# Optimization experiments

Hardware: AMD Instinct MI355X
Metric: run time of the kernel (lower is better)

The kernel has to match this reference:

```python
import jax, jax.numpy as jnp
import numpy as np

H = 16       # num_attention_heads
HKV = 4      # num_key_value_heads
HD = 128     # head_dim
G = H // HKV # num_key_value_groups


def setup_inputs() -> dict:
    key = jax.random.key(0)
    ks = jax.random.split(key, 7)
    s = 0.02
    B, S, D = 2, 2048, 2048
    return {
        "hidden_states": jax.random.normal(ks[0], (B, S, D), jnp.float32),
        "Wq": jax.random.normal(ks[1], (D, H * HD), jnp.float32) * s,
        "Wk": jax.random.normal(ks[2], (D, HKV * HD), jnp.float32) * s,
        "Wv": jax.random.normal(ks[3], (D, HKV * HD), jnp.float32) * s,
        "Wg": jax.random.normal(ks[4], (H * HD, HKV), jnp.float32) * s,
        "Wd": jax.random.normal(ks[5], (HKV * HD, HKV), jnp.float32) * s,
        "Wo": jax.random.normal(ks[6], (H * HD, D), jnp.float32) * s,
    }


def reference(hidden_states, Wq, Wk, Wv, Wg, Wd, Wo):
    b, s, _ = hidden_states.shape
    scale = HD ** -0.5

    q_flat = hidden_states @ Wq                    # [b,s,H*HD]
    k_flat = hidden_states @ Wk                    # [b,s,HKV*HD]
    v_flat = hidden_states @ Wv                    # [b,s,HKV*HD]

    gate = q_flat @ Wg                             # [b,s,HKV] (per query pos)
    delta = v_flat @ Wd                            # [b,s,HKV] (per key pos)
    # attn_bias: [b,HKV,key_len] after transpose; broadcast over query dim
    bias = (jax.nn.sigmoid(gate) * delta).transpose(0, 2, 1)  # [b,HKV,s]

    # [b,HKV,G,s,HD] query grouped by kv-head; [b,HKV,s,HD] key/value
    q = q_flat.reshape(b, s, HKV, G, HD).transpose(0, 2, 3, 1, 4)
    k = k_flat.reshape(b, s, HKV, HD).transpose(0, 2, 1, 3)
    v = v_flat.reshape(b, s, HKV, HD).transpose(0, 2, 1, 3)

    scores = jnp.einsum('bngqd,bnkd->bngqk', q, k) * scale  # [b,HKV,G,s,s]
    logits = scores + bias[:, :, None, None, :]

    causal = jnp.tril(jnp.ones((s, s), dtype=bool))
    # 'relu' mask: key positions allowed only where relu(bias) > 0
    allowed = causal[None, None, None] & (bias > 0)[:, :, None, None, :]
    neg = jnp.finfo(logits.dtype).min
    logits = jnp.where(allowed, logits, neg)

    p = jax.nn.softmax(logits, axis=-1)
    o = jnp.einsum('bngqk,bnkd->bngqd', p, v)               # [b,HKV,G,s,HD]
    o = o.transpose(0, 3, 1, 2, 4).reshape(b, s, H * HD)
    return o @ Wo
```

## Files before the change

kernel.cpp:

```cpp
#include <hip/hip_runtime.h>
#include <hip/hip_bf16.h>
#include <cmath>
#include <cstdint>

typedef __attribute__((ext_vector_type(8))) short short8;
typedef __attribute__((ext_vector_type(4))) float floatx4;
typedef __attribute__((ext_vector_type(4))) unsigned int uintx4;

typedef const __attribute__((address_space(1))) unsigned int* gas_p;
typedef __attribute__((address_space(3))) unsigned int* las_p;

#define LOG2E 1.4426950408889634f

__device__ inline unsigned short f2bf(float f) {
  unsigned int u = __builtin_bit_cast(unsigned int, f);
  unsigned int r = (u + 0x7FFFu + ((u >> 16) & 1u)) >> 16;
  return (unsigned short)r;
}
__device__ inline float bf2f(unsigned short h) {
  unsigned int u = ((unsigned int)h) << 16;
  return __builtin_bit_cast(float, u);
}

__global__ void k_f32_to_bf16(const float* __restrict__ in, unsigned short* __restrict__ out, int n4) {
  int i = blockIdx.x * 256 + threadIdx.x;
  if (i >= n4) return;
  float4 v = reinterpret_cast<const float4*>(in)[i];
  uint2 o;
  o.x = (unsigned)f2bf(v.x) | ((unsigned)f2bf(v.y) << 16);
  o.y = (unsigned)f2bf(v.z) | ((unsigned)f2bf(v.w) << 16);
  reinterpret_cast<uint2*>(out)[i] = o;
}

__global__ void k_transpose_w(const float* __restrict__ in, unsigned short* __restrict__ out,
                              int K, int N, float scl) {
  __shared__ float t[32][33];
  int n0 = blockIdx.x * 32, k0 = blockIdx.y * 32;
  int tx = threadIdx.x & 31, ty = threadIdx.x >> 5;
  #pragma unroll
  for (int r = ty; r < 32; r += 8)
    t[r][tx] = in[(long)(k0 + r) * N + n0 + tx];
  __syncthreads();
  #pragma unroll
  for (int r = ty; r < 32; r += 8)
    out[(long)(n0 + r) * K + k0 + tx] = f2bf(t[tx][r] * scl);
}

__global__ void k_wproj(const float* __restrict__ W, const float* __restrict__ Ws,
                        float* __restrict__ out, int Kw) {
  int d = blockIdx.x;
  float a0 = 0, a1 = 0, a2 = 0, a3 = 0;
  for (int j = threadIdx.x; j < Kw; j += 256) {
    float w = W[(long)d * Kw + j];
    float4 g = reinterpret_cast<const float4*>(Ws)[j];
    a0 += w * g.x; a1 += w * g.y; a2 += w * g.z; a3 += w * g.w;
  }
  #pragma unroll
  for (int off = 1; off < 64; off <<= 1) {
    a0 += __shfl_xor(a0, off, 64); a1 += __shfl_xor(a1, off, 64);
    a2 += __shfl_xor(a2, off, 64); a3 += __shfl_xor(a3, off, 64);
  }
  __shared__ float red[4][4];
  if ((threadIdx.x & 63) == 0) {
    int wv = threadIdx.x >> 6;
    red[wv][0] = a0; red[wv][1] = a1; red[wv][2] = a2; red[wv][3] = a3;
  }
  __syncthreads();
  if (threadIdx.x < 4) {
    int nn = threadIdx.x;
    out[d * 4 + nn] = red[0][nn] + red[1][nn] + red[2][nn] + red[3][nn];
  }
}

__global__ void k_bias(const float* __restrict__ hs, const float* __restrict__ Wqg,
                       const float* __restrict__ Wvd, float* __restrict__ bias) {
  int row = blockIdx.x;
  int b = row >> 11, s = row & 2047;
  float g0 = 0, g1 = 0, g2 = 0, g3 = 0, d0 = 0, d1 = 0, d2 = 0, d3 = 0;
  const float* h = hs + (long)row * 2048;
  for (int j = threadIdx.x; j < 2048; j += 256) {
    float x = h[j];
    float4 a = reinterpret_cast<const float4*>(Wqg)[j];
    float4 c = reinterpret_cast<const float4*>(Wvd)[j];
    g0 += x * a.x; g1 += x * a.y; g2 += x * a.z; g3 += x * a.w;
    d0 += x * c.x; d1 += x * c.y; d2 += x * c.z; d3 += x * c.w;
  }
  #pragma unroll
  for (int off = 1; off < 64; off <<= 1) {
    g0 += __shfl_xor(g0, off, 64); g1 += __shfl_xor(g1, off, 64);
    g2 += __shfl_xor(g2, off, 64); g3 += __shfl_xor(g3, off, 64);
    d0 += __shfl_xor(d0, off, 64); d1 += __shfl_xor(d1, off, 64);
    d2 += __shfl_xor(d2, off, 64); d3 += __shfl_xor(d3, off, 64);
  }
  __shared__ float red[4][8];
  if ((threadIdx.x & 63) == 0) {
    int wv = threadIdx.x >> 6;
    red[wv][0] = g0; red[wv][1] = g1; red[wv][2] = g2; red[wv][3] = g3;
    red[wv][4] = d0; red[wv][5] = d1; red[wv][6] = d2; red[wv][7] = d3;
  }
  __syncthreads();
  if (threadIdx.x < 4) {
    int nn = threadIdx.x;
    float gg = red[0][nn] + red[1][nn] + red[2][nn] + red[3][nn];
    float dd = red[0][4 + nn] + red[1][4 + nn] + red[2][4 + nn] + red[3][4 + nn];
    float sig = 1.0f / (1.0f + __expf(-gg));
    float v = sig * dd;
    bias[(b * 4 + nn) * 2048 + s] = (v > 0.0f) ? v * LOG2E : -INFINITY;
  }
}

template <int WRITE_BF16>
__global__ __launch_bounds__(256, 2) void k_gemm_bt(
    const unsigned short* __restrict__ A, const unsigned short* __restrict__ Bt,
    void* __restrict__ Cout, int M, int N, int K) {
  __shared__ __align__(16) unsigned short As[128 * 32];
  __shared__ __align__(16) unsigned short Bs[128 * 32];
  const int tid = threadIdx.x;
  const int lane = tid & 63, wave = tid >> 6;
  const int quad = lane >> 4, l16 = lane & 15;
  const long bm = (long)blockIdx.y * 128, bn = (long)blockIdx.x * 128;
  const int wm = (wave >> 1) * 64, wn = (wave & 1) * 64;

  const floatx4 fz = {0.f, 0.f, 0.f, 0.f};
  floatx4 acc[4][4];
  #pragma unroll
  for (int i = 0; i < 4; i++)
    #pragma unroll
    for (int j = 0; j < 4; j++) acc[i][j] = fz;

  const int r0 = tid >> 2, c0 = (tid & 3) * 8;
  const unsigned short* Ag = A + (bm + r0) * K + c0;
  const unsigned short* Bg = Bt + (bn + r0) * K + c0;
  unsigned short* AsW0 = As + (wave * 16) * 32;
  unsigned short* AsW1 = As + (wave * 16 + 64) * 32;
  unsigned short* BsW0 = Bs + (wave * 16) * 32;
  unsigned short* BsW1 = Bs + (wave * 16 + 64) * 32;

  for (int kt = 0; kt < K; kt += 32) {
    __syncthreads();
    __builtin_amdgcn_global_load_lds((gas_p)(const void*)(Ag + kt),
                                     (las_p)(void*)AsW0, 16, 0, 0);
    __builtin_amdgcn_global_load_lds((gas_p)(const void*)(Ag + (long)64 * K + kt),
                                     (las_p)(void*)AsW1, 16, 0, 0);
    __builtin_amdgcn_global_load_lds((gas_p)(const void*)(Bg + kt),
                                     (las_p)(void*)BsW0, 16, 0, 0);
    __builtin_amdgcn_global_load_lds((gas_p)(const void*)(Bg + (long)64 * K + kt),
                                     (las_p)(void*)BsW1, 16, 0, 0);
    __syncthreads();
    short8 af[4], bf[4];
    #pragma unroll
    for (int i = 0; i < 4; i++)
      af[i] = *reinterpret_cast<const short8*>(&As[(wm + i * 16 + l16) * 32 + quad * 8]);
    #pragma unroll
    for (int j = 0; j < 4; j++)
      bf[j] = *reinterpret_cast<const short8*>(&Bs[(wn + j * 16 + l16) * 32 + quad * 8]);
    #pragma unroll
    for (int i = 0; i < 4; i++)
      #pragma unroll
      for (int j = 0; j < 4; j++)
        acc[i][j] = __builtin_amdgcn_mfma_f32_16x16x32_bf16(af[i], bf[j], acc[i][j], 0, 0, 0);
  }
  #pragma unroll
  for (int i = 0; i < 4; i++)
    #pragma unroll
    for (int j = 0; j < 4; j++)
      #pragma unroll
      for (int r = 0; r < 4; r++) {
        const long row = bm + wm + i * 16 + quad * 4 + r;
        const long col = bn + wn + j * 16 + l16;
        const float v = acc[i][j][r];
        if (WRITE_BF16)
          ((unsigned short*)Cout)[row * N + col] = f2bf(v);
        else
          ((float*)Cout)[row * N + col] = v;
      }
}

__global__ void k_transpose_v(const unsigned short* __restrict__ qkv, unsigned short* __restrict__ vt) {
  __shared__ unsigned short t[32][33];
  int c0 = blockIdx.x * 32, s0 = blockIdx.y * 32, b = blockIdx.z;
  int tx = threadIdx.x & 31, ty = threadIdx.x >> 5;
  #pragma unroll
  for (int r = ty; r < 32; r += 8)
    t[r][tx] = qkv[((long)(b * 2048 + s0 + r)) * 3072 + 2560 + c0 + tx];
  __syncthreads();
  #pragma unroll
  for (int r = ty; r < 32; r += 8)
    vt[((long)(b * 512 + c0 + r)) * 2048 + s0 + tx] = t[tx][r];
}

__global__ void k_vmean2(const unsigned short* __restrict__ vT, float* __restrict__ vmean) {
  const int row = blockIdx.x;
  const int tid = threadIdx.x, lane = tid & 63, wave = tid >> 6;
  uintx4 v = reinterpret_cast<const uintx4*>(vT + (long)row * 2048)[tid];
  float s = 0.f;
  #pragma unroll
  for (int i = 0; i < 4; i++) {
    unsigned u = v[i];
    s += bf2f((unsigned short)(u & 0xffff)) + bf2f((unsigned short)(u >> 16));
  }
  #pragma unroll
  for (int off = 1; off < 64; off <<= 1) s += __shfl_xor(s, off, 64);
  __shared__ float red[4];
  if (lane == 0) red[wave] = s;
  __syncthreads();
  if (tid == 0) vmean[row] = (red[0] + red[1] + red[2] + red[3]) * (1.0f / 2048.0f);
}

__global__ __launch_bounds__(256, 3) void k_attn(
    const unsigned short* __restrict__ qkv,
    const float* __restrict__ biasb,
    const unsigned short* __restrict__ vT,
    const float* __restrict__ vmean,
    unsigned short* __restrict__ o)
{
  int idx = blockIdx.x;
  const int g = idx & 3;
  const int n = (idx >> 2) & 3;
  const int b = (idx >> 4) & 1;
  const int qt = 31 - (idx >> 5);
  const int tid = threadIdx.x, lane = tid & 63, wave = tid >> 6;
  const int quad = lane >> 4, l16 = lane & 15;
  const int q0 = qt * 64 + wave * 16;

  __shared__ __align__(16) unsigned short Ks[64 * 144];
  __shared__ __align__(16) unsigned short Vs[128 * 72];
  __shared__ __align__(16) unsigned short Ps[4 * 16 * 72];
  unsigned short* Psw = Ps + wave * 1152;

  short8 qf[4];
  {
    const unsigned short* qp = qkv + (long)(b * 2048) * 3072 + (n * 4 + g) * 128;
    #pragma unroll
    for (int ks = 0; ks < 4; ks++)
      qf[ks] = *reinterpret_cast<const short8*>(
          qp + (long)(q0 + l16) * 3072 + ks * 32 + quad * 8);
  }

  const floatx4 fz = {0.f, 0.f, 0.f, 0.f};
  floatx4 oacc[8];
  #pragma unroll
  for (int j = 0; j < 8; j++) oacc[j] = fz;
  float mrow = -INFINITY, lrow = 0.0f;

  const float* biasrow = biasb + (b * 4 + n) * 2048;
  const unsigned short* kbase = qkv + (long)(b * 2048) * 3072 + 2048 + n * 128;
  const unsigned short* vbase = vT + (long)(b * 512 + n * 128) * 2048;
  const int kk_ = tid >> 4, hdo_ = (tid & 15) * 8;
  const int hd_ = tid >> 3, ko_ = (tid & 7) * 8;

  uintx4 kreg[4], vreg[4];
  float4 breg[4];
  {
    const unsigned short* kp = kbase;
    const unsigned short* vp = vbase;
    #pragma unroll
    for (int it = 0; it < 4; it++)
      kreg[it] = *reinterpret_cast<const uintx4*>(kp + (long)(kk_ + it * 16) * 3072 + hdo_);
    #pragma unroll
    for (int it = 0; it < 4; it++)
      vreg[it] = *reinterpret_cast<const uintx4*>(vp + (long)(hd_ + it * 32) * 2048 + ko_);
    #pragma unroll
    for (int kt = 0; kt < 4; kt++)
      breg[kt] = *reinterpret_cast<const float4*>(biasrow + kt * 16 + quad * 4);
  }

  const int kend = qt * 64 + 64;
  for (int k0 = 0; k0 < kend; k0 += 64) {
    __syncthreads();
    #pragma unroll
    for (int it = 0; it < 4; it++)
      *reinterpret_cast<uintx4*>(&Ks[(kk_ + it * 16) * 144 + hdo_]) = kreg[it];
    #pragma unroll
    for (int it = 0; it < 4; it++)
      *reinterpret_cast<uintx4*>(&Vs[(hd_ + it * 32) * 72 + ko_]) = vreg[it];
    float4 bcur[4];
    #pragma unroll
    for (int kt = 0; kt < 4; kt++) bcur[kt] = breg[kt];

    if (k0 + 64 < kend) {
      const unsigned short* kp = kbase + (long)(k0 + 64) * 3072;
      const unsigned short* vp = vbase + (k0 + 64);
      #pragma unroll
      for (int it = 0; it < 4; it++)
        kreg[it] = *reinterpret_cast<const uintx4*>(kp + (long)(kk_ + it * 16) * 3072 + hdo_);
      #pragma unroll
      for (int it = 0; it < 4; it++)
        vreg[it] = *reinterpret_cast<const uintx4*>(vp + (long)(hd_ + it * 32) * 2048 + ko_);
      #pragma unroll
      for (int kt = 0; kt < 4; kt++)
        breg[kt] = *reinterpret_cast<const float4*>(biasrow + (k0 + 64) + kt * 16 + quad * 4);
    }
    __syncthreads();

    const bool active = (k0 <= q0 + 15);
    if (active) {
      floatx4 sacc[4];
      #pragma unroll
      for (int kt = 0; kt < 4; kt++)
        sacc[kt] = (floatx4){bcur[kt].x, bcur[kt].y, bcur[kt].z, bcur[kt].w};
      #pragma unroll
      for (int ks = 0; ks < 4; ks++) {
        short8 kf[4];
        #pragma unroll
        for (int kt = 0; kt < 4; kt++)
          kf[kt] = *reinterpret_cast<const short8*>(&Ks[(kt * 16 + l16) * 144 + ks * 32 + quad * 8]);
        #pragma unroll
        for (int kt = 0; kt < 4; kt++)
          sacc[kt] = __builtin_amdgcn_mfma_f32_16x16x32_bf16(kf[kt], qf[ks], sacc[kt], 0, 0, 0);
      }

      const bool full = (k0 + 63 <= q0);
      if (!full) {
        const int diff = (q0 + l16) - (k0 + quad * 4);
        #pragma unroll
        for (int kt = 0; kt < 4; kt++)
          #pragma unroll
          for (int r = 0; r < 4; r++)
            if (kt * 16 + r > diff) sacc[kt][r] = -INFINITY;
      }
      float mx = -INFINITY;
      #pragma unroll
      for (int kt = 0; kt < 4; kt++)
        #pragma unroll
        for (int r = 0; r < 4; r++) mx = fmaxf(mx, sacc[kt][r]);
      mx = fmaxf(mx, __shfl_xor(mx, 16, 64));
      mx = fmaxf(mx, __shfl_xor(mx, 32, 64));
      const float mn = fmaxf(mrow, mx);
      const float mnc = fmaxf(mn, -1e38f);
      const float alpha = __builtin_amdgcn_exp2f(mrow - mnc);
      float rs = 0.0f;
      unsigned pk[4][2];
      #pragma unroll
      for (int kt = 0; kt < 4; kt++) {
        #pragma unroll
        for (int r = 0; r < 4; r++) {
          float p = __builtin_amdgcn_exp2f(sacc[kt][r] - mnc);
          sacc[kt][r] = p;
          rs += p;
        }
        #pragma unroll
        for (int r2 = 0; r2 < 2; r2++)
          pk[kt][r2] = (unsigned)f2bf(sacc[kt][2 * r2]) | ((unsigned)f2bf(sacc[kt][2 * r2 + 1]) << 16);
      }
      rs += __shfl_xor(rs, 16, 64);
      rs += __shfl_xor(rs, 32, 64);
      mrow = mn;
      lrow = lrow * alpha + rs;

      float al[4];
      #pragma unroll
      for (int r = 0; r < 4; r++) al[r] = __shfl(alpha, quad * 4 + r, 64);
      #pragma unroll
      for (int j = 0; j < 8; j++)
        #pragma unroll
        for (int r = 0; r < 4; r++) oacc[j][r] *= al[r];

      unsigned* Pd = reinterpret_cast<unsigned*>(Psw);
      #pragma unroll
      for (int kt = 0; kt < 4; kt++)
        #pragma unroll
        for (int r2 = 0; r2 < 2; r2++)
          Pd[l16 * 36 + kt * 8 + quad * 2 + r2] = pk[kt][r2];

      #pragma unroll
      for (int ks2 = 0; ks2 < 2; ks2++) {
        short8 pf = *reinterpret_cast<const short8*>(&Psw[l16 * 72 + ks2 * 32 + quad * 8]);
        #pragma unroll
        for (int j = 0; j < 8; j++) {
          short8 vf = *reinterpret_cast<const short8*>(&Vs[(j * 16 + l16) * 72 + ks2 * 32 + quad * 8]);
          oacc[j] = __builtin_amdgcn_mfma_f32_16x16x32_bf16(pf, vf, oacc[j], 0, 0, 0);
        }
      }
    }
  }

  const long obase = (long)(b * 2048) * 2048 + (n * 4 + g) * 128;
  #pragma unroll
  for (int r = 0; r < 4; r++) {
    const int qrow = q0 + quad * 4 + r;
    const float l = __shfl(lrow, quad * 4 + r, 64);
    const float inv = (l > 0.0f) ? 1.0f / l : 0.0f;
    #pragma unroll
    for (int j = 0; j < 8; j++) {
      const int hd = j * 16 + l16;
      float v = oacc[j][r] * inv;
      if (l <= 0.0f) v = vmean[(b * 4 + n) * 128 + hd];
      o[obase + (long)qrow * 2048 + hd] = f2bf(v);
    }
  }
}

extern "C" void kernel_launch(void* const* d_in, const int* in_sizes, int n_in,
                              void* d_out, int out_size, void* d_ws, size_t ws_size,
                              hipStream_t stream) {
  const float* hs = (const float*)d_in[0];
  const float* Wq = (const float*)d_in[1];
  const float* Wk = (const float*)d_in[2];
  const float* Wv = (const float*)d_in[3];
  const float* Wg = (const float*)d_in[4];
  const float* Wd = (const float*)d_in[5];
  const float* Wo = (const float*)d_in[6];
  float* out = (float*)d_out;

  char* ws = (char*)d_ws;
  unsigned short* hsb   = (unsigned short*)(ws);
  unsigned short* Wcomb = (unsigned short*)(ws + 16777216);
  unsigned short* Wot   = (unsigned short*)(ws + 29360128);
  float*  Wqg   = (float*)(ws + 37748736);
  float*  Wvd   = (float*)(ws + 37781504);
  float*  biasb = (float*)(ws + 37814272);
  unsigned short* qkv = (unsigned short*)(ws + 37879808);
  unsigned short* vT  = (unsigned short*)(ws + 63045632);
  float*  vmean = (float*)(ws + 67239936);
  unsigned short* ob  = (unsigned short*)(ws + 67244032);

  const float QSCALE = 0.08838834764831845f * LOG2E;

  k_f32_to_bf16<<<2097152 / 256, 256, 0, stream>>>(hs, hsb, 2097152);

  {
    dim3 g1(2048 / 32, 2048 / 32);
    dim3 g2(512 / 32, 2048 / 32);
    k_transpose_w<<<g1, 256, 0, stream>>>(Wq, Wcomb, 2048, 2048, QSCALE);
    k_transpose_w<<<g2, 256, 0, stream>>>(Wk, Wcomb + (long)2048 * 2048, 2048, 512, 1.0f);
    k_transpose_w<<<g2, 256, 0, stream>>>(Wv, Wcomb + (long)2560 * 2048, 2048, 512, 1.0f);
    k_transpose_w<<<g1, 256, 0, stream>>>(Wo, Wot, 2048, 2048, 1.0f);
  }

  k_wproj<<<2048, 256, 0, stream>>>(Wq, Wg, Wqg, 2048);
  k_wproj<<<2048, 256, 0, stream>>>(Wv, Wd, Wvd, 512);

  k_bias<<<4096, 256, 0, stream>>>(hs, Wqg, Wvd, biasb);

  {
    dim3 gq(3072 / 128, 4096 / 128);
    k_gemm_bt<1><<<gq, 256, 0, stream>>>(hsb, Wcomb, qkv, 4096, 3072, 2048);
  }

  {
    dim3 gv(16, 64, 2);
    k_transpose_v<<<gv, 256, 0, stream>>>(qkv, vT);
  }

  k_vmean2<<<1024, 256, 0, stream>>>(vT, vmean);

  k_attn<<<1024, 256, 0, stream>>>(qkv, biasb, vT, vmean, ob);

  {
    dim3 go(2048 / 128, 4096 / 128);
    k_gemm_bt<0><<<go, 256, 0, stream>>>(ob, Wot, out, 4096, 2048, 2048);
  }
}
```

Measured before the change: 344.4 us.

## Merge prep kernels and enlarge attention blocks to 128 query rows

Folds the four weight-transpose launches into one kernel and the two weight-projection launches into another. It also fuses the fp32-to-bf16 conversion of hidden states into the bias kernel so hidden states are read once. The attention kernel now uses 512-thread blocks of 8 waves covering 128 query rows, sharing each K/V tile load across twice as many waves and changing the K shared-memory padding. The risk is more idle waves per block on causal diagonal tiles, and register pressure under the new launch bounds.

```diff
diff --git a/kernel.cpp b/kernel.cpp
--- a/kernel.cpp
+++ b/kernel.cpp
@@ -22,33 +22,37 @@
   return __builtin_bit_cast(float, u);
 }
 
-__global__ void k_f32_to_bf16(const float* __restrict__ in, unsigned short* __restrict__ out, int n4) {
-  int i = blockIdx.x * 256 + threadIdx.x;
-  if (i >= n4) return;
-  float4 v = reinterpret_cast<const float4*>(in)[i];
-  uint2 o;
-  o.x = (unsigned)f2bf(v.x) | ((unsigned)f2bf(v.y) << 16);
-  o.y = (unsigned)f2bf(v.z) | ((unsigned)f2bf(v.w) << 16);
-  reinterpret_cast<uint2*>(out)[i] = o;
-}
-
-__global__ void k_transpose_w(const float* __restrict__ in, unsigned short* __restrict__ out,
-                              int K, int N, float scl) {
+__global__ void k_transpose_all(const float* __restrict__ Wq, const float* __restrict__ Wk,
+                                const float* __restrict__ Wv, const float* __restrict__ Wo,
+                                unsigned short* __restrict__ Wcomb, unsigned short* __restrict__ Wot,
+                                float qscale) {
   __shared__ float t[32][33];
-  int n0 = blockIdx.x * 32, k0 = blockIdx.y * 32;
-  int tx = threadIdx.x & 31, ty = threadIdx.x >> 5;
+  int id = blockIdx.x;
+  const float* src; unsigned short* dst; int N; float scl = 1.0f;
+  if (id < 4096)        { src = Wq; dst = Wcomb;                     N = 2048; scl = qscale; }
+  else if (id < 5120)   { src = Wk; dst = Wcomb + (long)2048 * 2048; N = 512;  id -= 4096; }
+  else if (id < 6144)   { src = Wv; dst = Wcomb + (long)2560 * 2048; N = 512;  id -= 5120; }
+  else                  { src = Wo; dst = Wot;                       N = 2048; id -= 6144; }
+  const int tilesX = N >> 5;
+  const int n0 = (id % tilesX) * 32, k0 = (id / tilesX) * 32;
+  const int tx = threadIdx.x & 31, ty = threadIdx.x >> 5;
   #pragma unroll
   for (int r = ty; r < 32; r += 8)
-    t[r][tx] = in[(long)(k0 + r) * N + n0 + tx];
+    t[r][tx] = src[(long)(k0 + r) * N + n0 + tx];
   __syncthreads();
   #pragma unroll
   for (int r = ty; r < 32; r += 8)
-    out[(long)(n0 + r) * K + k0 + tx] = f2bf(t[tx][r] * scl);
-}
-
-__global__ void k_wproj(const float* __restrict__ W, const float* __restrict__ Ws,
-                        float* __restrict__ out, int Kw) {
-  int d = blockIdx.x;
+    dst[(long)(n0 + r) * 2048 + k0 + tx] = f2bf(t[tx][r] * scl);
+}
+
+__global__ void k_wproj2(const float* __restrict__ Wq, const float* __restrict__ Wg,
+                         const float* __restrict__ Wv, const float* __restrict__ Wd,
+                         float* __restrict__ Wqg, float* __restrict__ Wvd) {
+  const int which = blockIdx.x >> 11, d = blockIdx.x & 2047;
+  const float* W  = which ? Wv : Wq;
+  const float* Ws = which ? Wd : Wg;
+  float* out      = which ? Wvd : Wqg;
+  const int Kw    = which ? 512 : 2048;
   float a0 = 0, a1 = 0, a2 = 0, a3 = 0;
   for (int j = threadIdx.x; j < Kw; j += 256) {
     float w = W[(long)d * Kw + j];
@@ -72,14 +76,27 @@
   }
 }
 
-__global__ void k_bias(const float* __restrict__ hs, const float* __restrict__ Wqg,
-                       const float* __restrict__ Wvd, float* __restrict__ bias) {
-  int row = blockIdx.x;
-  int b = row >> 11, s = row & 2047;
+__global__ void k_biascvt(const float* __restrict__ hs, const float* __restrict__ Wqg,
+                          const float* __restrict__ Wvd, unsigned short* __restrict__ hsb,
+                          float* __restrict__ bias) {
+  const int row = blockIdx.x;
+  const int b = row >> 11, s = row & 2047;
+  const int tid = threadIdx.x;
+  const float* h = hs + (long)row * 2048;
+  float4 h0 = reinterpret_cast<const float4*>(h)[tid * 2];
+  float4 h1 = reinterpret_cast<const float4*>(h)[tid * 2 + 1];
+  uintx4 pkv;
+  pkv[0] = (unsigned)f2bf(h0.x) | ((unsigned)f2bf(h0.y) << 16);
+  pkv[1] = (unsigned)f2bf(h0.z) | ((unsigned)f2bf(h0.w) << 16);
+  pkv[2] = (unsigned)f2bf(h1.x) | ((unsigned)f2bf(h1.y) << 16);
+  pkv[3] = (unsigned)f2bf(h1.z) | ((unsigned)f2bf(h1.w) << 16);
+  reinterpret_cast<uintx4*>(hsb + (long)row * 2048)[tid] = pkv;
   float g0 = 0, g1 = 0, g2 = 0, g3 = 0, d0 = 0, d1 = 0, d2 = 0, d3 = 0;
-  const float* h = hs + (long)row * 2048;
-  for (int j = threadIdx.x; j < 2048; j += 256) {
-    float x = h[j];
+  const float hx[8] = {h0.x, h0.y, h0.z, h0.w, h1.x, h1.y, h1.z, h1.w};
+  #pragma unroll
+  for (int i = 0; i < 8; i++) {
+    const int j = tid * 8 + i;
+    float x = hx[i];
     float4 a = reinterpret_cast<const float4*>(Wqg)[j];
     float4 c = reinterpret_cast<const float4*>(Wvd)[j];
     g0 += x * a.x; g1 += x * a.y; g2 += x * a.z; g3 += x * a.w;
@@ -93,14 +110,14 @@
     d2 += __shfl_xor(d2, off, 64); d3 += __shfl_xor(d3, off, 64);
   }
   __shared__ float red[4][8];
-  if ((threadIdx.x & 63) == 0) {
-    int wv = threadIdx.x >> 6;
+  if ((tid & 63) == 0) {
+    int wv = tid >> 6;
     red[wv][0] = g0; red[wv][1] = g1; red[wv][2] = g2; red[wv][3] = g3;
     red[wv][4] = d0; red[wv][5] = d1; red[wv][6] = d2; red[wv][7] = d3;
   }
   __syncthreads();
-  if (threadIdx.x < 4) {
-    int nn = threadIdx.x;
+  if (tid < 4) {
+    int nn = tid;
     float gg = red[0][nn] + red[1][nn] + red[2][nn] + red[3][nn];
     float dd = red[0][4 + nn] + red[1][4 + nn] + red[2][4 + nn] + red[3][4 + nn];
     float sig = 1.0f / (1.0f + __expf(-gg));
@@ -207,7 +224,7 @@
   if (tid == 0) vmean[row] = (red[0] + red[1] + red[2] + red[3]) * (1.0f / 2048.0f);
 }
 
-__global__ __launch_bounds__(256, 3) void k_attn(
+__global__ __launch_bounds__(512, 4) void k_attn(
     const unsigned short* __restrict__ qkv,
     const float* __restrict__ biasb,
     const unsigned short* __restrict__ vT,
@@ -218,14 +235,14 @@
   const int g = idx & 3;
   const int n = (idx >> 2) & 3;
   const int b = (idx >> 4) & 1;
-  const int qt = 31 - (idx >> 5);
+  const int qt = 15 - (idx >> 5);
   const int tid = threadIdx.x, lane = tid & 63, wave = tid >> 6;
   const int quad = lane >> 4, l16 = lane & 15;
-  const int q0 = qt * 64 + wave * 16;
-
-  __shared__ __align__(16) unsigned short Ks[64 * 144];
+  const int q0 = qt * 128 + wave * 16;
+
+  __shared__ __align__(16) unsigned short Ks[64 * 136];
   __shared__ __align__(16) unsigned short Vs[128 * 72];
-  __shared__ __align__(16) unsigned short Ps[4 * 16 * 72];
+  __shared__ __align__(16) unsigned short Ps[8 * 16 * 72];
   unsigned short* Psw = Ps + wave * 1152;
 
   short8 qf[4];
@@ -249,31 +266,29 @@
   const int kk_ = tid >> 4, hdo_ = (tid & 15) * 8;
   const int hd_ = tid >> 3, ko_ = (tid & 7) * 8;
 
-  uintx4 kreg[4], vreg[4];
+  uintx4 kreg[2], vreg[2];
   float4 breg[4];
   {
-    const unsigned short* kp = kbase;
-    const unsigned short* vp = vbase;
-    #pragma unroll
-    for (int it = 0; it < 4; it++)
-      kreg[it] = *reinterpret_cast<const uintx4*>(kp + (long)(kk_ + it * 16) * 3072 + hdo_);
-    #pragma unroll
-    for (int it = 0; it < 4; it++)
-      vreg[it] = *reinterpret_cast<const uintx4*>(vp + (long)(hd_ + it * 32) * 2048 + ko_);
+    #pragma unroll
+    for (int it = 0; it < 2; it++)
+      kreg[it] = *reinterpret_cast<const uintx4*>(kbase + (long)(kk_ + it * 32) * 3072 + hdo_);
+    #pragma unroll
+    for (int it = 0; it < 2; it++)
+      vreg[it] = *reinterpret_cast<const uintx4*>(vbase + (long)(hd_ + it * 64) * 2048 + ko_);
     #pragma unroll
     for (int kt = 0; kt < 4; kt++)
       breg[kt] = *reinterpret_cast<const float4*>(biasrow + kt * 16 + quad * 4);
   }
 
-  const int kend = qt * 64 + 64;
+  const int kend = qt * 128 + 128;
   for (int k0 = 0; k0 < kend; k0 += 64) {
     __syncthreads();
     #pragma unroll
-    for (int it = 0; it < 4; it++)
-      *reinterpret_cast<uintx4*>(&Ks[(kk_ + it * 16) * 144 + hdo_]) = kreg[it];
-    #pragma unroll
-    for (int it = 0; it < 4; it++)
-      *reinterpret_cast<uintx4*>(&Vs[(hd_ + it * 32) * 72 + ko_]) = vreg[it];
+    for (int it = 0; it < 2; it++)
+      *reinterpret_cast<uintx4*>(&Ks[(kk_ + it * 32) * 136 + hdo_]) = kreg[it];
+    #pragma unroll
+    for (int it = 0; it < 2; it++)
+      *reinterpret_cast<uintx4*>(&Vs[(hd_ + it * 64) * 72 + ko_]) = vreg[it];
     float4 bcur[4];
     #pragma unroll
     for (int kt = 0; kt < 4; kt++) bcur[kt] = breg[kt];
@@ -282,11 +297,11 @@
       const unsigned short* kp = kbase + (long)(k0 + 64) * 3072;
       const unsigned short* vp = vbase + (k0 + 64);
       #pragma unroll
-      for (int it = 0; it < 4; it++)
-        kreg[it] = *reinterpret_cast<const uintx4*>(kp + (long)(kk_ + it * 16) * 3072 + hdo_);
-      #pragma unroll
-      for (int it = 0; it < 4; it++)
-        vreg[it] = *reinterpret_cast<const uintx4*>(vp + (long)(hd_ + it * 32) * 2048 + ko_);
+      for (int it = 0; it < 2; it++)
+        kreg[it] = *reinterpret_cast<const uintx4*>(kp + (long)(kk_ + it * 32) * 3072 + hdo_);
+      #pragma unroll
+      for (int it = 0; it < 2; it++)
+        vreg[it] = *reinterpret_cast<const uintx4*>(vp + (long)(hd_ + it * 64) * 2048 + ko_);
       #pragma unroll
       for (int kt = 0; kt < 4; kt++)
         breg[kt] = *reinterpret_cast<const float4*>(biasrow + (k0 + 64) + kt * 16 + quad * 4);
@@ -304,7 +319,7 @@
         short8 kf[4];
         #pragma unroll
         for (int kt = 0; kt < 4; kt++)
-          kf[kt] = *reinterpret_cast<const short8*>(&Ks[(kt * 16 + l16) * 144 + ks * 32 + quad * 8]);
+          kf[kt] = *reinterpret_cast<const short8*>(&Ks[(kt * 16 + l16) * 136 + ks * 32 + quad * 8]);
         #pragma unroll
         for (int kt = 0; kt < 4; kt++)
           sacc[kt] = __builtin_amdgcn_mfma_f32_16x16x32_bf16(kf[kt], qf[ks], sacc[kt], 0, 0, 0);
@@ -417,21 +432,11 @@
 
   const float QSCALE = 0.08838834764831845f * LOG2E;
 
-  k_f32_to_bf16<<<2097152 / 256, 256, 0, stream>>>(hs, hsb, 2097152);
-
-  {
-    dim3 g1(2048 / 32, 2048 / 32);
-    dim3 g2(512 / 32, 2048 / 32);
-    k_transpose_w<<<g1, 256, 0, stream>>>(Wq, Wcomb, 2048, 2048, QSCALE);
-    k_transpose_w<<<g2, 256, 0, stream>>>(Wk, Wcomb + (long)2048 * 2048, 2048, 512, 1.0f);
-    k_transpose_w<<<g2, 256, 0, stream>>>(Wv, Wcomb + (long)2560 * 2048, 2048, 512, 1.0f);
-    k_transpose_w<<<g1, 256, 0, stream>>>(Wo, Wot, 2048, 2048, 1.0f);
-  }
-
-  k_wproj<<<2048, 256, 0, stream>>>(Wq, Wg, Wqg, 2048);
-  k_wproj<<<2048, 256, 0, stream>>>(Wv, Wd, Wvd, 512);
-
-  k_bias<<<4096, 256, 0, stream>>>(hs, Wqg, Wvd, biasb);
+  k_wproj2<<<4096, 256, 0, stream>>>(Wq, Wg, Wv, Wd, Wqg, Wvd);
+
+  k_transpose_all<<<10240, 256, 0, stream>>>(Wq, Wk, Wv, Wo, Wcomb, Wot, QSCALE);
+
+  k_biascvt<<<4096, 256, 0, stream>>>(hs, Wqg, Wvd, hsb, biasb);
 
   {
     dim3 gq(3072 / 128, 4096 / 128);
@@ -445,7 +450,7 @@
 
   k_vmean2<<<1024, 256, 0, stream>>>(vT, vmean);
 
-  k_attn<<<1024, 256, 0, stream>>>(qkv, biasb, vT, vmean, ob);
+  k_attn<<<512, 512, 0, stream>>>(qkv, biasb, vT, vmean, ob);
 
   {
     dim3 go(2048 / 128, 4096 / 128);
```

New measurement: 381.2 us. +10.7%, slower.
